# Performance work log

Measured on AMD Instinct MI355X. Metric: run time of the kernel, lower is better.

The kernel has to match this reference:

```python
import jax, jax.numpy as jnp
import numpy as np

B, S, H = 8, 2048, 1024
W_SCALE = 0.02  # small init keeps the 2048-step recurrence numerically stable


def setup_inputs() -> dict:
    key = jax.random.key(0)
    ks = jax.random.split(key, 6)
    x = jax.random.normal(ks[0], (B, S, H), dtype=jnp.float32)
    h0 = jnp.zeros((B, H), dtype=jnp.float32)
    # torch Linear y = x @ W.T + b; we store pre-transposed [in, out] matrices
    W_in = jax.random.normal(ks[1], (H, 3 * H), dtype=jnp.float32) * W_SCALE
    b_in = jnp.zeros((3 * H,), dtype=jnp.float32)
    W_gate = jax.random.normal(ks[2], (H, 2 * H), dtype=jnp.float32) * W_SCALE
    b_gate = jnp.zeros((2 * H,), dtype=jnp.float32)
    W_rec = jax.random.normal(ks[3], (H, H), dtype=jnp.float32) * W_SCALE
    b_rec = jnp.zeros((H,), dtype=jnp.float32)
    W_out = jax.random.normal(ks[4], (H, H), dtype=jnp.float32) * W_SCALE
    b_out = jnp.zeros((H,), dtype=jnp.float32)
    return {"x": x, "h0": h0, "W_in": W_in, "b_in": b_in,
            "W_gate": W_gate, "b_gate": b_gate, "W_rec": W_rec, "b_rec": b_rec,
            "W_out": W_out, "b_out": b_out}


def reference(x, h0, W_in, b_in, W_gate, b_gate, W_rec, b_rec, W_out, b_out):
    # input projection, chunk into u, v, w and activate (swish)
    feats = x @ W_in + b_in                      # [B,S,3H]
    u, v, w = jnp.split(feats, 3, axis=-1)
    drive = jax.nn.silu(u) * jax.nn.silu(v) + w  # (1-gate) branch, [B,S,H]

    def step(h, d_t):
        g = h @ W_gate + b_gate                  # [B,2H]
        gv, gt = jnp.split(g, 2, axis=-1)
        gate = jax.nn.sigmoid(gv) * jax.nn.silu(gt)  # GLU gate
        new_h = gate * (h @ W_rec + b_rec) + (1.0 - gate) * d_t
        # dropout is identity in eval mode
        return new_h, new_h

    final_h, hs = jax.lax.scan(step, h0, jnp.swapaxes(drive, 0, 1))  # hs: [S,B,H]
    hs = jnp.swapaxes(hs, 0, 1)                  # [B,S,H]
    out = hs @ W_out + b_out                     # per-timestep output_proj, batched
    return out, final_h
```

## Files before the change

kernel.cpp:

```cpp
#include <hip/hip_runtime.h>

typedef short short8 __attribute__((ext_vector_type(8)));
typedef __bf16 bf16x8 __attribute__((ext_vector_type(8)));
typedef float f32x4 __attribute__((ext_vector_type(4)));
typedef float f32x4v __attribute__((ext_vector_type(4)));
typedef unsigned short u16x4 __attribute__((ext_vector_type(4)));
typedef unsigned int uint2v __attribute__((ext_vector_type(2)));
typedef unsigned long long u64;

__device__ __forceinline__ unsigned short f2b(float f) {
  unsigned x = __builtin_bit_cast(unsigned, f);
  x = x + 0x7fffu + ((x >> 16) & 1u);
  return (unsigned short)(x >> 16);
}
__device__ __forceinline__ float b2f(unsigned short u) {
  unsigned x = ((unsigned)u) << 16;
  return __builtin_bit_cast(float, x);
}
__device__ __forceinline__ f32x4 mfma16(short8 a, short8 b, f32x4 c) {
  return __builtin_amdgcn_mfma_f32_16x16x32_bf16(
      __builtin_bit_cast(bf16x8, a), __builtin_bit_cast(bf16x8, b), c, 0, 0, 0);
}
typedef const __attribute__((address_space(1))) void* gas_p;
typedef __attribute__((address_space(3))) void* las_p;
__device__ __forceinline__ void gload_lds16(const void* g, void* l) {
  __builtin_amdgcn_global_load_lds((gas_p)g, (las_p)l, 16, 0, 0);
}

__global__ __launch_bounds__(256) void k_cvt_bf16(const float* __restrict__ in,
                                                  unsigned short* __restrict__ out,
                                                  int n4) {
  int i = blockIdx.x * 256 + threadIdx.x;
  if (i >= n4) return;
  f32x4v v = *(const f32x4v*)(in + (size_t)i * 4);
  u16x4 o;
  o[0] = f2b(v[0]); o[1] = f2b(v[1]); o[2] = f2b(v[2]); o[3] = f2b(v[3]);
  *(u16x4*)(out + (size_t)i * 4) = o;
}

__global__ __launch_bounds__(256) void k_init_hq(const float* __restrict__ h0,
                                                 unsigned int* __restrict__ hq) {
  int idx = blockIdx.x * 256 + threadIdx.x;
  if (idx >= 8192) return;
  int b = idx >> 10, i = idx & 1023;
  hq[(size_t)b * 2048 + i] = (unsigned int)f2b(h0[idx]);
  hq[(size_t)b * 2048 + 1024 + i] = 0u;
}

__global__ __launch_bounds__(256) void k_transpose_bf16(const float* __restrict__ in,
                                                        unsigned short* __restrict__ out,
                                                        int R, int C) {
  __shared__ unsigned short tile[32][33];
  int c0 = blockIdx.x * 32, r0 = blockIdx.y * 32;
  int tx = threadIdx.x & 31, ty = threadIdx.x >> 5;
#pragma unroll
  for (int i = 0; i < 4; i++) {
    int r = ty + i * 8;
    tile[r][tx] = f2b(in[(size_t)(r0 + r) * C + c0 + tx]);
  }
  __syncthreads();
#pragma unroll
  for (int i = 0; i < 4; i++) {
    int rr = ty + i * 8;
    out[(size_t)(c0 + rr) * R + r0 + tx] = tile[tx][rr];
  }
}

__global__ __launch_bounds__(256) void k_gemm_drive(const unsigned short* __restrict__ xb,
                                                    const unsigned short* __restrict__ WinT,
                                                    const float* __restrict__ b_in,
                                                    unsigned short* __restrict__ drive) {
  __shared__ unsigned short At[128 * 32];
  __shared__ unsigned short Bt[3][64 * 32];
  const int tid = threadIdx.x;
  const int w = tid >> 6, l = tid & 63;
  const int wm = w >> 1, wn = w & 1;
  const int lr = l & 15, lk = (l >> 4) * 8;
  const int m0 = blockIdx.x * 128;
  const int j0 = blockIdx.y * 64;
  f32x4 acc[3][4][2];
#pragma unroll
  for (int s = 0; s < 3; s++)
#pragma unroll
    for (int mi = 0; mi < 4; mi++)
#pragma unroll
      for (int ni = 0; ni < 2; ni++)
#pragma unroll
        for (int e = 0; e < 4; e++) acc[s][mi][ni][e] = 0.f;

  const int sr = tid >> 2;
  const int skb = (tid & 3) * 8;
  for (int kt = 0; kt < 32; kt++) {
    const int k0 = kt * 32;
    gload_lds16(xb + (size_t)(m0 + sr) * 1024 + k0 + skb, &At[w * 512]);
    gload_lds16(xb + (size_t)(m0 + 64 + sr) * 1024 + k0 + skb, &At[2048 + w * 512]);
#pragma unroll
    for (int s = 0; s < 3; s++)
      gload_lds16(WinT + (size_t)(s * 1024 + j0 + sr) * 1024 + k0 + skb, &Bt[s][w * 512]);
    __syncthreads();
    short8 Af[4], Bf[3][2];
#pragma unroll
    for (int mi = 0; mi < 4; mi++)
      Af[mi] = *(const short8*)&At[(wm * 64 + mi * 16 + lr) * 32 + lk];
#pragma unroll
    for (int s = 0; s < 3; s++)
#pragma unroll
      for (int ni = 0; ni < 2; ni++)
        Bf[s][ni] = *(const short8*)&Bt[s][(wn * 32 + ni * 16 + lr) * 32 + lk];
#pragma unroll
    for (int s = 0; s < 3; s++)
#pragma unroll
      for (int mi = 0; mi < 4; mi++)
#pragma unroll
        for (int ni = 0; ni < 2; ni++)
          acc[s][mi][ni] = mfma16(Af[mi], Bf[s][ni], acc[s][mi][ni]);
    __syncthreads();
  }
#pragma unroll
  for (int ni = 0; ni < 2; ni++) {
    const int c = j0 + wn * 32 + ni * 16 + lr;
    const float bu = b_in[c], bv = b_in[1024 + c], bw = b_in[2048 + c];
#pragma unroll
    for (int mi = 0; mi < 4; mi++) {
      const int r0 = m0 + wm * 64 + mi * 16 + (l >> 4) * 4;
#pragma unroll
      for (int e = 0; e < 4; e++) {
        float u = acc[0][mi][ni][e] + bu;
        float v = acc[1][mi][ni][e] + bv;
        float wv = acc[2][mi][ni][e] + bw;
        float su = u / (1.f + __expf(-u));
        float sv = v / (1.f + __expf(-v));
        drive[(size_t)(r0 + e) * 1024 + c] = f2b(su * sv + wv);
      }
    }
  }
}

__global__ __launch_bounds__(1024, 4) void k_scan(const unsigned short* __restrict__ WgT,
                                                  const unsigned short* __restrict__ WrT,
                                                  const float* __restrict__ b_gate,
                                                  const float* __restrict__ b_rec,
                                                  const unsigned short* __restrict__ drive,
                                                  unsigned int* __restrict__ hq,
                                                  unsigned short* __restrict__ hs,
                                                  float* __restrict__ final_h) {
  const int g = blockIdx.x;
  const int b = g >> 5;
  const int s = g & 31;
  const int tid = threadIdx.x;
  const int w = tid >> 6, l = tid & 63;

  __shared__ unsigned int tileh[512];
  __shared__ float buf[4][3][32];

  const int mat = w >> 2, kq = w & 3;
  const int lr = l & 15, ko = l >> 4;
  const bool av = (lr == 0);
  short8 Breg[2][8];
  if (w < 12) {
    const unsigned short* WT = (mat == 2) ? WrT : WgT;
    const int rowbase = ((mat == 1) ? 1024 : 0) + s * 32;
#pragma unroll
    for (int tile = 0; tile < 2; ++tile)
#pragma unroll
      for (int ks = 0; ks < 8; ++ks)
        Breg[tile][ks] = *(const short8*)&WT[(size_t)(rowbase + tile * 16 + lr) * 1024 +
                                             kq * 256 + ks * 32 + ko * 8];
  }

  const bool isld = tid >= 768;
  const int q = tid - 768;

  const bool isfin = tid < 32;
  const int fcol = s * 32 + tid;
  float bgv = 0.f, bgt = 0.f, brc = 0.f;
  if (isfin) { bgv = b_gate[fcol]; bgt = b_gate[1024 + fcol]; brc = b_rec[fcol]; }

  for (int t = 0; t < 2048; ++t) {
    const int p = t & 1;
    unsigned short dpf = 0;
    if (isfin) dpf = drive[(size_t)(b * 2048 + t) * 1024 + fcol];

    if (isld) {
      const unsigned tg = (unsigned)t;
      const u64* hb = (const u64*)(hq + (size_t)(b * 2 + p) * 1024);
      u64 v0 = 0, v1 = 0;
      unsigned pend = 3u;
      do {
        if (pend & 1u)
          v0 = __hip_atomic_load(hb + 2 * q, __ATOMIC_RELAXED,
                                 __HIP_MEMORY_SCOPE_AGENT);
        if (pend & 2u)
          v1 = __hip_atomic_load(hb + 2 * q + 1, __ATOMIC_RELAXED,
                                 __HIP_MEMORY_SCOPE_AGENT);
        unsigned np = 0;
        if ((((unsigned)v0 >> 16) != tg) | (((unsigned)(v0 >> 32) >> 16) != tg))
          np |= 1u;
        if ((((unsigned)v1 >> 16) != tg) | (((unsigned)(v1 >> 32) >> 16) != tg))
          np |= 2u;
        pend = np;
      } while (pend);
      uint2v pk;
      pk[0] = __builtin_amdgcn_perm((unsigned)(v0 >> 32), (unsigned)v0, 0x05040100u);
      pk[1] = __builtin_amdgcn_perm((unsigned)(v1 >> 32), (unsigned)v1, 0x05040100u);
      *(uint2v*)&tileh[2 * q] = pk;
    }
    __syncthreads();

    if (w < 12) {
      f32x4 a0, a1;
#pragma unroll
      for (int e = 0; e < 4; ++e) { a0[e] = 0.f; a1[e] = 0.f; }
      const char* base = (const char*)tileh + kq * 512 + ko * 16;
#pragma unroll
      for (int ks = 0; ks < 8; ++ks) {
        short8 Af;
#pragma unroll
        for (int e = 0; e < 8; ++e) Af[e] = 0;
        if (av) Af = *(const short8*)(base + ks * 64);
        a0 = mfma16(Af, Breg[0][ks], a0);
        a1 = mfma16(Af, Breg[1][ks], a1);
      }
      if (l < 16) {
        buf[kq][mat][l] = a0[0];
        buf[kq][mat][16 + l] = a1[0];
      }
    }
    __syncthreads();

    if (isfin) {
      const float gv = ((buf[0][0][tid] + buf[1][0][tid]) +
                        (buf[2][0][tid] + buf[3][0][tid])) + bgv;
      const float gt = ((buf[0][1][tid] + buf[1][1][tid]) +
                        (buf[2][1][tid] + buf[3][1][tid])) + bgt;
      const float rc = ((buf[0][2][tid] + buf[1][2][tid]) +
                        (buf[2][2][tid] + buf[3][2][tid])) + brc;
      const float sgv = 1.f / (1.f + __expf(-gv));
      const float sgt = 1.f / (1.f + __expf(-gt));
      const float gate = sgv * gt * sgt;
      const float nh = gate * rc + (1.f - gate) * b2f(dpf);
      const unsigned short nhb = f2b(nh);
      __hip_atomic_store(hq + (size_t)(b * 2 + (p ^ 1)) * 1024 + fcol,
                         (((unsigned)(t + 1)) << 16) | (unsigned)nhb,
                         __ATOMIC_RELAXED, __HIP_MEMORY_SCOPE_AGENT);
      hs[(size_t)(b * 2048 + t) * 1024 + fcol] = nhb;
      if (t == 2047) final_h[b * 1024 + fcol] = nh;
    }
  }
}

__global__ __launch_bounds__(256) void k_gemm_out(const unsigned short* __restrict__ hs,
                                                  const unsigned short* __restrict__ WoT,
                                                  const float* __restrict__ b_out,
                                                  float* __restrict__ out) {
  __shared__ unsigned short At[128 * 32];
  __shared__ unsigned short Bt[128 * 32];
  const int tid = threadIdx.x;
  const int w = tid >> 6, l = tid & 63;
  const int wm = w >> 1, wn = w & 1;
  const int lr = l & 15, lk = (l >> 4) * 8;
  const int m0 = blockIdx.x * 128;
  const int n0 = blockIdx.y * 128;
  f32x4 acc[4][4];
#pragma unroll
  for (int mi = 0; mi < 4; mi++)
#pragma unroll
    for (int ni = 0; ni < 4; ni++)
#pragma unroll
      for (int e = 0; e < 4; e++) acc[mi][ni][e] = 0.f;

  const int sr = tid >> 2;
  const int skb = (tid & 3) * 8;
  for (int kt = 0; kt < 32; kt++) {
    const int k0 = kt * 32;
    gload_lds16(hs + (size_t)(m0 + sr) * 1024 + k0 + skb, &At[w * 512]);
    gload_lds16(hs + (size_t)(m0 + 64 + sr) * 1024 + k0 + skb, &At[2048 + w * 512]);
    gload_lds16(WoT + (size_t)(n0 + sr) * 1024 + k0 + skb, &Bt[w * 512]);
    gload_lds16(WoT + (size_t)(n0 + 64 + sr) * 1024 + k0 + skb, &Bt[2048 + w * 512]);
    __syncthreads();
    short8 Af[4], Bf[4];
#pragma unroll
    for (int mi = 0; mi < 4; mi++)
      Af[mi] = *(const short8*)&At[(wm * 64 + mi * 16 + lr) * 32 + lk];
#pragma unroll
    for (int ni = 0; ni < 4; ni++)
      Bf[ni] = *(const short8*)&Bt[(wn * 64 + ni * 16 + lr) * 32 + lk];
#pragma unroll
    for (int mi = 0; mi < 4; mi++)
#pragma unroll
      for (int ni = 0; ni < 4; ni++)
        acc[mi][ni] = mfma16(Af[mi], Bf[ni], acc[mi][ni]);
    __syncthreads();
  }
#pragma unroll
  for (int ni = 0; ni < 4; ni++) {
    const int c = n0 + wn * 64 + ni * 16 + lr;
    const float bo = b_out[c];
#pragma unroll
    for (int mi = 0; mi < 4; mi++) {
      const int r0 = m0 + wm * 64 + mi * 16 + (l >> 4) * 4;
#pragma unroll
      for (int e = 0; e < 4; e++)
        out[(size_t)(r0 + e) * 1024 + c] = acc[mi][ni][e] + bo;
    }
  }
}

extern "C" void kernel_launch(void* const* d_in, const int* in_sizes, int n_in,
                              void* d_out, int out_size, void* d_ws, size_t ws_size,
                              hipStream_t stream) {
  const float* x      = (const float*)d_in[0];
  const float* h0     = (const float*)d_in[1];
  const float* W_in   = (const float*)d_in[2];
  const float* b_in   = (const float*)d_in[3];
  const float* W_gate = (const float*)d_in[4];
  const float* b_gate = (const float*)d_in[5];
  const float* W_rec  = (const float*)d_in[6];
  const float* b_rec  = (const float*)d_in[7];
  const float* W_out  = (const float*)d_in[8];
  const float* b_out  = (const float*)d_in[9];
  float* outp = (float*)d_out;

  size_t off = 0;
  auto alloc = [&](size_t bytes) {
    void* p = (char*)d_ws + off;
    off += (bytes + 255) & ~(size_t)255;
    return p;
  };
  unsigned short* xb    = (unsigned short*)alloc((size_t)16777216 * 2);
  unsigned short* WinT  = (unsigned short*)alloc((size_t)3072 * 1024 * 2);
  unsigned short* WgT   = (unsigned short*)alloc((size_t)2048 * 1024 * 2);
  unsigned short* WrT   = (unsigned short*)alloc((size_t)1024 * 1024 * 2);
  unsigned short* WoT   = (unsigned short*)alloc((size_t)1024 * 1024 * 2);
  unsigned short* drive = (unsigned short*)alloc((size_t)16777216 * 2);
  unsigned short* hs    = (unsigned short*)alloc((size_t)16777216 * 2);
  unsigned int*   hq    = (unsigned int*)alloc((size_t)8 * 2 * 1024 * 4);

  k_cvt_bf16<<<16384, 256, 0, stream>>>(x, xb, 4194304);
  k_transpose_bf16<<<dim3(96, 32), 256, 0, stream>>>(W_in, WinT, 1024, 3072);
  k_transpose_bf16<<<dim3(64, 32), 256, 0, stream>>>(W_gate, WgT, 1024, 2048);
  k_transpose_bf16<<<dim3(32, 32), 256, 0, stream>>>(W_rec, WrT, 1024, 1024);
  k_transpose_bf16<<<dim3(32, 32), 256, 0, stream>>>(W_out, WoT, 1024, 1024);
  k_init_hq<<<32, 256, 0, stream>>>(h0, hq);

  k_gemm_drive<<<dim3(128, 16), 256, 0, stream>>>(xb, WinT, b_in, drive);
  k_scan<<<256, 1024, 0, stream>>>(WgT, WrT, b_gate, b_rec, drive, hq, hs,
                                   outp + 16777216);
  k_gemm_out<<<dim3(128, 8), 256, 0, stream>>>(hs, WoT, b_out, outp);
}
```

Baseline: 4.051 ms.

## Group scan blocks per batch on one XCD and poll hidden state with sc0 loads

Each scan block reads its hardware XCC ID and claims a (batch, slice) slot through per-XCD atomic counters, so all 32 blocks of one batch row tend to land on the same XCD. A startup handshake with timeouts then tests whether sc0 (L2-coherent, not system-scope) loads and stores see each other's updates, and the blocks vote on it. If the vote passes, the per-step hidden-state exchange uses a fast mirror buffer with cheaper sc0 polling instead of agent-scope atomics. It falls back to the original agent-scope path on timeout. This adds startup handshake cost, extra stores on every step, and relies on timing-based detection of coherence.

```diff
diff --git a/kernel.cpp b/kernel.cpp
--- a/kernel.cpp
+++ b/kernel.cpp
@@ -25,6 +25,17 @@
 typedef __attribute__((address_space(3))) void* las_p;
 __device__ __forceinline__ void gload_lds16(const void* g, void* l) {
   __builtin_amdgcn_global_load_lds((gas_p)g, (las_p)l, 16, 0, 0);
+}
+
+__device__ __forceinline__ void load2_sc0(const u64* p0, const u64* p1,
+                                          u64& v0, u64& v1) {
+  asm volatile("global_load_dwordx2 %0, %2, off sc0\n\t"
+               "global_load_dwordx2 %1, %3, off sc0\n\t"
+               "s_waitcnt vmcnt(0)"
+               : "=v"(v0), "=v"(v1) : "v"(p0), "v"(p1) : "memory");
+}
+__device__ __forceinline__ void store_sc0(unsigned* p, unsigned v) {
+  asm volatile("global_store_dword %0, %1, off sc0" :: "v"(p), "v"(v) : "memory");
 }
 
 __global__ __launch_bounds__(256) void k_cvt_bf16(const float* __restrict__ in,
@@ -39,12 +50,18 @@
 }
 
 __global__ __launch_bounds__(256) void k_init_hq(const float* __restrict__ h0,
-                                                 unsigned int* __restrict__ hq) {
+                                                 unsigned int* __restrict__ hq,
+                                                 unsigned int* __restrict__ fq) {
   int idx = blockIdx.x * 256 + threadIdx.x;
   if (idx >= 8192) return;
   int b = idx >> 10, i = idx & 1023;
-  hq[(size_t)b * 2048 + i] = (unsigned int)f2b(h0[idx]);
-  hq[(size_t)b * 2048 + 1024 + i] = 0u;
+  unsigned v = (unsigned)f2b(h0[idx]);
+  hq[(size_t)b * 2048 + i] = v;       hq[(size_t)b * 2048 + 1024 + i] = 0u;
+  fq[(size_t)b * 2048 + i] = v;       fq[(size_t)b * 2048 + 1024 + i] = 0u;
+}
+
+__global__ void k_zero16(unsigned int* __restrict__ p) {
+  if (threadIdx.x < 16) p[threadIdx.x] = 0u;
 }
 
 __global__ __launch_bounds__(256) void k_transpose_bf16(const float* __restrict__ in,
@@ -142,16 +159,36 @@
                                                   const float* __restrict__ b_rec,
                                                   const unsigned short* __restrict__ drive,
                                                   unsigned int* __restrict__ hq,
+                                                  unsigned int* __restrict__ fq,
+                                                  unsigned int* __restrict__ tst,
+                                                  unsigned int* __restrict__ cnt,
+                                                  unsigned int* __restrict__ vote,
                                                   unsigned short* __restrict__ hs,
                                                   float* __restrict__ final_h) {
-  const int g = blockIdx.x;
-  const int b = g >> 5;
-  const int s = g & 31;
   const int tid = threadIdx.x;
   const int w = tid >> 6, l = tid & 63;
 
+  __shared__ unsigned int claim_sh;
+  __shared__ int lds_ok;
   __shared__ unsigned int tileh[512];
   __shared__ float buf[4][3][32];
+
+  if (tid == 0) {
+    unsigned xcd;
+    asm volatile("s_getreg_b32 %0, hwreg(HW_REG_XCC_ID)" : "=s"(xcd));
+    xcd &= 7u;
+    unsigned ring = 0, slot = 0;
+    for (int k = 0; k < 8; ++k) {
+      ring = (xcd + (unsigned)k) & 7u;
+      slot = atomicAdd(&cnt[ring], 1u);
+      if (slot < 32u) break;
+    }
+    claim_sh = (ring << 16) | slot;
+    lds_ok = 1;
+  }
+  __syncthreads();
+  const int b = (int)(claim_sh >> 16);
+  const int s = (int)(claim_sh & 0xffffu);
 
   const int mat = w >> 2, kq = w & 3;
   const int lr = l & 15, ko = l >> 4;
@@ -170,12 +207,51 @@
 
   const bool isld = tid >= 768;
   const int q = tid - 768;
-
   const bool isfin = tid < 32;
   const int fcol = s * 32 + tid;
   float bgv = 0.f, bgt = 0.f, brc = 0.f;
   if (isfin) { bgv = b_gate[fcol]; bgt = b_gate[1024 + fcol]; brc = b_rec[fcol]; }
 
+  {
+    bool tok = true;
+    for (int r = 1; r <= 6; ++r) {
+      const int tp = r & 1;
+      const unsigned rtag = 0xE000u + (unsigned)r;
+      if (isfin)
+        store_sc0(tst + ((size_t)(b * 2 + tp) << 10) + fcol, (rtag << 16) | 1u);
+      if (isld && tok) {
+        const u64* w0 = (const u64*)(tst + ((size_t)(b * 2 + tp) << 10)) + 2 * q;
+        const u64 t0r = __builtin_amdgcn_s_memrealtime();
+        for (;;) {
+          u64 v0, v1;
+          load2_sc0(w0, w0 + 1, v0, v1);
+          const bool ok = (((unsigned)v0 >> 16) == rtag) &
+                          (((unsigned)(v0 >> 32) >> 16) == rtag) &
+                          (((unsigned)v1 >> 16) == rtag) &
+                          (((unsigned)(v1 >> 32) >> 16) == rtag);
+          if (ok) break;
+          if (__builtin_amdgcn_s_memrealtime() - t0r > 20000) { tok = false; break; }
+        }
+      }
+      __syncthreads();
+    }
+    if (isld && !tok) lds_ok = 0;
+    __syncthreads();
+    if (tid == 0) {
+      const unsigned my = 0x10000u | (unsigned)lds_ok;
+      (void)__hip_atomic_fetch_add(&vote[b], my, __ATOMIC_RELAXED,
+                                   __HIP_MEMORY_SCOPE_AGENT);
+      unsigned vv;
+      do {
+        vv = __hip_atomic_load(&vote[b], __ATOMIC_RELAXED, __HIP_MEMORY_SCOPE_AGENT);
+      } while ((vv >> 16) < 32u);
+      claim_sh = ((vv & 0xffffu) == 32u) ? 1u : 0u;
+    }
+    __syncthreads();
+  }
+  const bool rok = (claim_sh != 0u);
+  bool mir = !rok;
+
   for (int t = 0; t < 2048; ++t) {
     const int p = t & 1;
     unsigned short dpf = 0;
@@ -183,23 +259,36 @@
 
     if (isld) {
       const unsigned tg = (unsigned)t;
-      const u64* hb = (const u64*)(hq + (size_t)(b * 2 + p) * 1024);
       u64 v0 = 0, v1 = 0;
-      unsigned pend = 3u;
-      do {
-        if (pend & 1u)
-          v0 = __hip_atomic_load(hb + 2 * q, __ATOMIC_RELAXED,
-                                 __HIP_MEMORY_SCOPE_AGENT);
-        if (pend & 2u)
-          v1 = __hip_atomic_load(hb + 2 * q + 1, __ATOMIC_RELAXED,
-                                 __HIP_MEMORY_SCOPE_AGENT);
-        unsigned np = 0;
-        if ((((unsigned)v0 >> 16) != tg) | (((unsigned)(v0 >> 32) >> 16) != tg))
-          np |= 1u;
-        if ((((unsigned)v1 >> 16) != tg) | (((unsigned)(v1 >> 32) >> 16) != tg))
-          np |= 2u;
-        pend = np;
-      } while (pend);
+      if (!mir) {
+        const u64* f0 = (const u64*)(fq + (size_t)(b * 2 + p) * 1024) + 2 * q;
+        const u64 t0r = __builtin_amdgcn_s_memrealtime();
+        for (;;) {
+          load2_sc0(f0, f0 + 1, v0, v1);
+          const bool ok = (((unsigned)v0 >> 16) == tg) &
+                          (((unsigned)(v0 >> 32) >> 16) == tg) &
+                          (((unsigned)v1 >> 16) == tg) &
+                          (((unsigned)(v1 >> 32) >> 16) == tg);
+          if (ok) break;
+          if (__builtin_amdgcn_s_memrealtime() - t0r > 50000) { mir = true; break; }
+        }
+      }
+      if (mir) {
+        const u64* hb = (const u64*)(hq + (size_t)(b * 2 + p) * 1024) + 2 * q;
+        unsigned pend = 3u;
+        do {
+          if (pend & 1u)
+            v0 = __hip_atomic_load(hb, __ATOMIC_RELAXED, __HIP_MEMORY_SCOPE_AGENT);
+          if (pend & 2u)
+            v1 = __hip_atomic_load(hb + 1, __ATOMIC_RELAXED, __HIP_MEMORY_SCOPE_AGENT);
+          unsigned np = 0;
+          if ((((unsigned)v0 >> 16) != tg) | (((unsigned)(v0 >> 32) >> 16) != tg))
+            np |= 1u;
+          if ((((unsigned)v1 >> 16) != tg) | (((unsigned)(v1 >> 32) >> 16) != tg))
+            np |= 2u;
+          pend = np;
+        } while (pend);
+      }
       uint2v pk;
       pk[0] = __builtin_amdgcn_perm((unsigned)(v0 >> 32), (unsigned)v0, 0x05040100u);
       pk[1] = __builtin_amdgcn_perm((unsigned)(v1 >> 32), (unsigned)v1, 0x05040100u);
@@ -240,8 +329,10 @@
       const float gate = sgv * gt * sgt;
       const float nh = gate * rc + (1.f - gate) * b2f(dpf);
       const unsigned short nhb = f2b(nh);
-      __hip_atomic_store(hq + (size_t)(b * 2 + (p ^ 1)) * 1024 + fcol,
-                         (((unsigned)(t + 1)) << 16) | (unsigned)nhb,
+      const unsigned pkv = (((unsigned)(t + 1)) << 16) | (unsigned)nhb;
+      const size_t poff = (size_t)(b * 2 + (p ^ 1)) * 1024 + fcol;
+      if (rok) store_sc0(fq + poff, pkv);
+      __hip_atomic_store(hq + poff, pkv,
                          __ATOMIC_RELAXED, __HIP_MEMORY_SCOPE_AGENT);
       hs[(size_t)(b * 2048 + t) * 1024 + fcol] = nhb;
       if (t == 2047) final_h[b * 1024 + fcol] = nh;
@@ -335,16 +426,21 @@
   unsigned short* drive = (unsigned short*)alloc((size_t)16777216 * 2);
   unsigned short* hs    = (unsigned short*)alloc((size_t)16777216 * 2);
   unsigned int*   hq    = (unsigned int*)alloc((size_t)8 * 2 * 1024 * 4);
+  unsigned int*   fq    = (unsigned int*)alloc((size_t)8 * 2 * 1024 * 4);
+  unsigned int*   tst   = (unsigned int*)alloc((size_t)8 * 2 * 1024 * 4);
+  unsigned int*   cnt   = (unsigned int*)alloc((size_t)16 * 4);
+  unsigned int*   vote  = cnt + 8;
 
   k_cvt_bf16<<<16384, 256, 0, stream>>>(x, xb, 4194304);
   k_transpose_bf16<<<dim3(96, 32), 256, 0, stream>>>(W_in, WinT, 1024, 3072);
   k_transpose_bf16<<<dim3(64, 32), 256, 0, stream>>>(W_gate, WgT, 1024, 2048);
   k_transpose_bf16<<<dim3(32, 32), 256, 0, stream>>>(W_rec, WrT, 1024, 1024);
   k_transpose_bf16<<<dim3(32, 32), 256, 0, stream>>>(W_out, WoT, 1024, 1024);
-  k_init_hq<<<32, 256, 0, stream>>>(h0, hq);
+  k_init_hq<<<32, 256, 0, stream>>>(h0, hq, fq);
+  k_zero16<<<1, 16, 0, stream>>>(cnt);
 
   k_gemm_drive<<<dim3(128, 16), 256, 0, stream>>>(xb, WinT, b_in, drive);
-  k_scan<<<256, 1024, 0, stream>>>(WgT, WrT, b_gate, b_rec, drive, hq, hs,
-                                   outp + 16777216);
+  k_scan<<<256, 1024, 0, stream>>>(WgT, WrT, b_gate, b_rec, drive, hq, fq, tst,
+                                   cnt, vote, hs, outp + 16777216);
   k_gemm_out<<<dim3(128, 8), 256, 0, stream>>>(hs, WoT, b_out, outp);
 }
```

New measurement: 4.629 ms. +14.3%, slower.

## Use 8-slot hidden-state ring with progress counters for scan block sync

Applied to the files above, without the earlier changes.

Replaces the double-buffered hidden-state exchange with an 8-deep ring buffer. A per-block progress array, checked by wave 0 before each store, bounds how far ahead any block can run. Without the ring, a block could overwrite a slot that a slower peer has not finished reading, so the ring and bound are meant to replace that implicit tighter coupling and reduce stalls between blocks. In exchange it adds a global progress poll, a sleep loop and an extra store every step, which could add latency to the critical path.

```diff
diff --git a/kernel.cpp b/kernel.cpp
--- a/kernel.cpp
+++ b/kernel.cpp
@@ -26,6 +26,8 @@
 __device__ __forceinline__ void gload_lds16(const void* g, void* l) {
   __builtin_amdgcn_global_load_lds((gas_p)g, (las_p)l, 16, 0, 0);
 }
+
+#define NPH 8
 
 __global__ __launch_bounds__(256) void k_cvt_bf16(const float* __restrict__ in,
                                                   unsigned short* __restrict__ out,
@@ -38,13 +40,19 @@
   *(u16x4*)(out + (size_t)i * 4) = o;
 }
 
-__global__ __launch_bounds__(256) void k_init_hq(const float* __restrict__ h0,
-                                                 unsigned int* __restrict__ hq) {
+__global__ __launch_bounds__(256) void k_init_hq8(const float* __restrict__ h0,
+                                                  unsigned int* __restrict__ hq) {
   int idx = blockIdx.x * 256 + threadIdx.x;
   if (idx >= 8192) return;
   int b = idx >> 10, i = idx & 1023;
-  hq[(size_t)b * 2048 + i] = (unsigned int)f2b(h0[idx]);
-  hq[(size_t)b * 2048 + 1024 + i] = 0u;
+  size_t base = (size_t)b * (NPH * 1024);
+  hq[base + i] = (unsigned int)f2b(h0[idx]);
+#pragma unroll
+  for (int s = 1; s < NPH; ++s) hq[base + s * 1024 + i] = 0u;
+}
+
+__global__ void k_zero_prog(unsigned int* __restrict__ p) {
+  if (threadIdx.x < 256) p[threadIdx.x] = 0u;
 }
 
 __global__ __launch_bounds__(256) void k_transpose_bf16(const float* __restrict__ in,
@@ -142,6 +150,7 @@
                                                   const float* __restrict__ b_rec,
                                                   const unsigned short* __restrict__ drive,
                                                   unsigned int* __restrict__ hq,
+                                                  unsigned int* __restrict__ prog,
                                                   unsigned short* __restrict__ hs,
                                                   float* __restrict__ final_h) {
   const int g = blockIdx.x;
@@ -177,13 +186,17 @@
   if (isfin) { bgv = b_gate[fcol]; bgt = b_gate[1024 + fcol]; brc = b_rec[fcol]; }
 
   for (int t = 0; t < 2048; ++t) {
-    const int p = t & 1;
     unsigned short dpf = 0;
     if (isfin) dpf = drive[(size_t)(b * 2048 + t) * 1024 + fcol];
 
+    unsigned ppv = 0u;
+    if (w == 0 && l >= 32)
+      ppv = __hip_atomic_load(prog + b * 32 + (l - 32), __ATOMIC_RELAXED,
+                              __HIP_MEMORY_SCOPE_AGENT);
+
     if (isld) {
       const unsigned tg = (unsigned)t;
-      const u64* hb = (const u64*)(hq + (size_t)(b * 2 + p) * 1024);
+      const u64* hb = (const u64*)(hq + ((size_t)(b * NPH + (t & 7)) << 10));
       u64 v0 = 0, v1 = 0;
       unsigned pend = 3u;
       do {
@@ -228,6 +241,17 @@
     }
     __syncthreads();
 
+    if (w == 0) {
+      bool pok = (l < 32) || ((int)ppv >= t - 6);
+      while (!__all(pok)) {
+        __builtin_amdgcn_s_sleep(1);
+        if (l >= 32)
+          ppv = __hip_atomic_load(prog + b * 32 + (l - 32), __ATOMIC_RELAXED,
+                                  __HIP_MEMORY_SCOPE_AGENT);
+        pok = (l < 32) || ((int)ppv >= t - 6);
+      }
+    }
+
     if (isfin) {
       const float gv = ((buf[0][0][tid] + buf[1][0][tid]) +
                         (buf[2][0][tid] + buf[3][0][tid])) + bgv;
@@ -240,11 +264,14 @@
       const float gate = sgv * gt * sgt;
       const float nh = gate * rc + (1.f - gate) * b2f(dpf);
       const unsigned short nhb = f2b(nh);
-      __hip_atomic_store(hq + (size_t)(b * 2 + (p ^ 1)) * 1024 + fcol,
+      __hip_atomic_store(hq + ((size_t)(b * NPH + ((t + 1) & 7)) << 10) + fcol,
                          (((unsigned)(t + 1)) << 16) | (unsigned)nhb,
                          __ATOMIC_RELAXED, __HIP_MEMORY_SCOPE_AGENT);
       hs[(size_t)(b * 2048 + t) * 1024 + fcol] = nhb;
       if (t == 2047) final_h[b * 1024 + fcol] = nh;
+      if (tid == 0)
+        __hip_atomic_store(prog + b * 32 + s, (unsigned)(t + 1),
+                           __ATOMIC_RELAXED, __HIP_MEMORY_SCOPE_AGENT);
     }
   }
 }
@@ -334,17 +361,19 @@
   unsigned short* WoT   = (unsigned short*)alloc((size_t)1024 * 1024 * 2);
   unsigned short* drive = (unsigned short*)alloc((size_t)16777216 * 2);
   unsigned short* hs    = (unsigned short*)alloc((size_t)16777216 * 2);
-  unsigned int*   hq    = (unsigned int*)alloc((size_t)8 * 2 * 1024 * 4);
+  unsigned int*   hq    = (unsigned int*)alloc((size_t)8 * NPH * 1024 * 4);
+  unsigned int*   prog  = (unsigned int*)alloc((size_t)256 * 4);
 
   k_cvt_bf16<<<16384, 256, 0, stream>>>(x, xb, 4194304);
   k_transpose_bf16<<<dim3(96, 32), 256, 0, stream>>>(W_in, WinT, 1024, 3072);
   k_transpose_bf16<<<dim3(64, 32), 256, 0, stream>>>(W_gate, WgT, 1024, 2048);
   k_transpose_bf16<<<dim3(32, 32), 256, 0, stream>>>(W_rec, WrT, 1024, 1024);
   k_transpose_bf16<<<dim3(32, 32), 256, 0, stream>>>(W_out, WoT, 1024, 1024);
-  k_init_hq<<<32, 256, 0, stream>>>(h0, hq);
+  k_init_hq8<<<32, 256, 0, stream>>>(h0, hq);
+  k_zero_prog<<<1, 256, 0, stream>>>(prog);
 
   k_gemm_drive<<<dim3(128, 16), 256, 0, stream>>>(xb, WinT, b_in, drive);
-  k_scan<<<256, 1024, 0, stream>>>(WgT, WrT, b_gate, b_rec, drive, hq, hs,
-                                   outp + 16777216);
+  k_scan<<<256, 1024, 0, stream>>>(WgT, WrT, b_gate, b_rec, drive, hq, prog,
+                                   hs, outp + 16777216);
   k_gemm_out<<<dim3(128, 8), 256, 0, stream>>>(hs, WoT, b_out, outp);
 }
```

Result: slower. 4.358 ms (+7.6%).

## Process two batch rows per scan block, halving the scan grid

Applied to the files above, without the earlier changes.

Each scan block now handles two batch rows, interleaving their recurrence steps within each timestep and reusing the same register-resident weight slices for both rows. The grid drops from 256 to 128 blocks, so fewer blocks take part in the cross-block spin-wait handoff and each weight slice is loaded once for two rows. In exchange, each block runs two serialized sync chains per timestep, so per-step latency roughly doubles inside a block. The intent is that one row's wait on the other blocks can overlap with work on the other row.

```diff
diff --git a/kernel.cpp b/kernel.cpp
--- a/kernel.cpp
+++ b/kernel.cpp
@@ -145,13 +145,13 @@
                                                   unsigned short* __restrict__ hs,
                                                   float* __restrict__ final_h) {
   const int g = blockIdx.x;
-  const int b = g >> 5;
+  const int r = g >> 5;
   const int s = g & 31;
   const int tid = threadIdx.x;
   const int w = tid >> 6, l = tid & 63;
 
-  __shared__ unsigned int tileh[512];
-  __shared__ float buf[4][3][32];
+  __shared__ unsigned int tileh[2][512];
+  __shared__ float buf[2][4][3][32];
 
   const int mat = w >> 2, kq = w & 3;
   const int lr = l & 15, ko = l >> 4;
@@ -178,73 +178,81 @@
 
   for (int t = 0; t < 2048; ++t) {
     const int p = t & 1;
-    unsigned short dpf = 0;
-    if (isfin) dpf = drive[(size_t)(b * 2048 + t) * 1024 + fcol];
-
-    if (isld) {
-      const unsigned tg = (unsigned)t;
-      const u64* hb = (const u64*)(hq + (size_t)(b * 2 + p) * 1024);
-      u64 v0 = 0, v1 = 0;
-      unsigned pend = 3u;
-      do {
-        if (pend & 1u)
-          v0 = __hip_atomic_load(hb + 2 * q, __ATOMIC_RELAXED,
-                                 __HIP_MEMORY_SCOPE_AGENT);
-        if (pend & 2u)
-          v1 = __hip_atomic_load(hb + 2 * q + 1, __ATOMIC_RELAXED,
-                                 __HIP_MEMORY_SCOPE_AGENT);
-        unsigned np = 0;
-        if ((((unsigned)v0 >> 16) != tg) | (((unsigned)(v0 >> 32) >> 16) != tg))
-          np |= 1u;
-        if ((((unsigned)v1 >> 16) != tg) | (((unsigned)(v1 >> 32) >> 16) != tg))
-          np |= 2u;
-        pend = np;
-      } while (pend);
-      uint2v pk;
-      pk[0] = __builtin_amdgcn_perm((unsigned)(v0 >> 32), (unsigned)v0, 0x05040100u);
-      pk[1] = __builtin_amdgcn_perm((unsigned)(v1 >> 32), (unsigned)v1, 0x05040100u);
-      *(uint2v*)&tileh[2 * q] = pk;
+    unsigned short dpf[2] = {0, 0};
+    if (isfin) {
+      dpf[0] = drive[(size_t)((2 * r) * 2048 + t) * 1024 + fcol];
+      dpf[1] = drive[(size_t)((2 * r + 1) * 2048 + t) * 1024 + fcol];
     }
-    __syncthreads();
-
-    if (w < 12) {
-      f32x4 a0, a1;
-#pragma unroll
-      for (int e = 0; e < 4; ++e) { a0[e] = 0.f; a1[e] = 0.f; }
-      const char* base = (const char*)tileh + kq * 512 + ko * 16;
-#pragma unroll
-      for (int ks = 0; ks < 8; ++ks) {
-        short8 Af;
-#pragma unroll
-        for (int e = 0; e < 8; ++e) Af[e] = 0;
-        if (av) Af = *(const short8*)(base + ks * 64);
-        a0 = mfma16(Af, Breg[0][ks], a0);
-        a1 = mfma16(Af, Breg[1][ks], a1);
+
+#pragma unroll
+    for (int ab = 0; ab < 2; ++ab) {
+      const int b = 2 * r + ab;
+
+      if (isld) {
+        const unsigned tg = (unsigned)t;
+        const u64* hb = (const u64*)(hq + (size_t)(b * 2 + p) * 1024);
+        u64 v0 = 0, v1 = 0;
+        unsigned pend = 3u;
+        do {
+          if (pend & 1u)
+            v0 = __hip_atomic_load(hb + 2 * q, __ATOMIC_RELAXED,
+                                   __HIP_MEMORY_SCOPE_AGENT);
+          if (pend & 2u)
+            v1 = __hip_atomic_load(hb + 2 * q + 1, __ATOMIC_RELAXED,
+                                   __HIP_MEMORY_SCOPE_AGENT);
+          unsigned np = 0;
+          if ((((unsigned)v0 >> 16) != tg) | (((unsigned)(v0 >> 32) >> 16) != tg))
+            np |= 1u;
+          if ((((unsigned)v1 >> 16) != tg) | (((unsigned)(v1 >> 32) >> 16) != tg))
+            np |= 2u;
+          pend = np;
+        } while (pend);
+        uint2v pk;
+        pk[0] = __builtin_amdgcn_perm((unsigned)(v0 >> 32), (unsigned)v0, 0x05040100u);
+        pk[1] = __builtin_amdgcn_perm((unsigned)(v1 >> 32), (unsigned)v1, 0x05040100u);
+        *(uint2v*)&tileh[ab][2 * q] = pk;
       }
-      if (l < 16) {
-        buf[kq][mat][l] = a0[0];
-        buf[kq][mat][16 + l] = a1[0];
+      __syncthreads();
+
+      if (w < 12) {
+        f32x4 a0, a1;
+#pragma unroll
+        for (int e = 0; e < 4; ++e) { a0[e] = 0.f; a1[e] = 0.f; }
+        const char* base = (const char*)&tileh[ab][0] + kq * 512 + ko * 16;
+#pragma unroll
+        for (int ks = 0; ks < 8; ++ks) {
+          short8 Af;
+#pragma unroll
+          for (int e = 0; e < 8; ++e) Af[e] = 0;
+          if (av) Af = *(const short8*)(base + ks * 64);
+          a0 = mfma16(Af, Breg[0][ks], a0);
+          a1 = mfma16(Af, Breg[1][ks], a1);
+        }
+        if (l < 16) {
+          buf[ab][kq][mat][l] = a0[0];
+          buf[ab][kq][mat][16 + l] = a1[0];
+        }
       }
-    }
-    __syncthreads();
-
-    if (isfin) {
-      const float gv = ((buf[0][0][tid] + buf[1][0][tid]) +
-                        (buf[2][0][tid] + buf[3][0][tid])) + bgv;
-      const float gt = ((buf[0][1][tid] + buf[1][1][tid]) +
-                        (buf[2][1][tid] + buf[3][1][tid])) + bgt;
-      const float rc = ((buf[0][2][tid] + buf[1][2][tid]) +
-                        (buf[2][2][tid] + buf[3][2][tid])) + brc;
-      const float sgv = 1.f / (1.f + __expf(-gv));
-      const float sgt = 1.f / (1.f + __expf(-gt));
-      const float gate = sgv * gt * sgt;
-      const float nh = gate * rc + (1.f - gate) * b2f(dpf);
-      const unsigned short nhb = f2b(nh);
-      __hip_atomic_store(hq + (size_t)(b * 2 + (p ^ 1)) * 1024 + fcol,
-                         (((unsigned)(t + 1)) << 16) | (unsigned)nhb,
-                         __ATOMIC_RELAXED, __HIP_MEMORY_SCOPE_AGENT);
-      hs[(size_t)(b * 2048 + t) * 1024 + fcol] = nhb;
-      if (t == 2047) final_h[b * 1024 + fcol] = nh;
+      __syncthreads();
+
+      if (isfin) {
+        const float gv = ((buf[ab][0][0][tid] + buf[ab][1][0][tid]) +
+                          (buf[ab][2][0][tid] + buf[ab][3][0][tid])) + bgv;
+        const float gt = ((buf[ab][0][1][tid] + buf[ab][1][1][tid]) +
+                          (buf[ab][2][1][tid] + buf[ab][3][1][tid])) + bgt;
+        const float rc = ((buf[ab][0][2][tid] + buf[ab][1][2][tid]) +
+                          (buf[ab][2][2][tid] + buf[ab][3][2][tid])) + brc;
+        const float sgv = 1.f / (1.f + __expf(-gv));
+        const float sgt = 1.f / (1.f + __expf(-gt));
+        const float gate = sgv * gt * sgt;
+        const float nh = gate * rc + (1.f - gate) * b2f(dpf[ab]);
+        const unsigned short nhb = f2b(nh);
+        __hip_atomic_store(hq + (size_t)(b * 2 + (p ^ 1)) * 1024 + fcol,
+                           (((unsigned)(t + 1)) << 16) | (unsigned)nhb,
+                           __ATOMIC_RELAXED, __HIP_MEMORY_SCOPE_AGENT);
+        hs[(size_t)(b * 2048 + t) * 1024 + fcol] = nhb;
+        if (t == 2047) final_h[b * 1024 + fcol] = nh;
+      }
     }
   }
 }
@@ -344,7 +352,7 @@
   k_init_hq<<<32, 256, 0, stream>>>(h0, hq);
 
   k_gemm_drive<<<dim3(128, 16), 256, 0, stream>>>(xb, WinT, b_in, drive);
-  k_scan<<<256, 1024, 0, stream>>>(WgT, WrT, b_gate, b_rec, drive, hq, hs,
-                                   outp + 16777216);
+  k_scan<<<128, 1024, 0, stream>>>(WgT, WrT, b_gate, b_rec, drive, hq,
+                                   hs, outp + 16777216);
   k_gemm_out<<<dim3(128, 8), 256, 0, stream>>>(hs, WoT, b_out, outp);
 }
```

Measured after the change: 5.029 ms. 24.1% more time.
